# Performance work log

Measured on AMD Instinct MI355X. Metric: run time of the kernel, lower is better.

## Reference

```python
import jax, jax.numpy as jnp
import numpy as np

BN_EPS = 1e-5

def _bn_relu(x, gamma, beta):
    # training-mode BatchNorm1d: biased batch stats over (B, N) per channel
    mean = x.mean(axis=(0, 2), keepdims=True)
    var = x.var(axis=(0, 2), keepdims=True)
    xn = (x - mean) * jax.lax.rsqrt(var + BN_EPS)
    return jax.nn.relu(xn * gamma[None, :, None] + beta[None, :, None])


def setup_inputs() -> dict:
    key = jax.random.key(0)
    ks = jax.random.split(key, 12)
    B, n1, n2, c1, c2 = 16, 4096, 1024, 128, 256
    in_ch, mlp = c1 + c2, [256, 128]
    xyz1 = jax.random.uniform(ks[0], (B, n1, 3), dtype=jnp.float32)
    xyz2 = jax.random.uniform(ks[1], (B, n2, 3), dtype=jnp.float32)
    feat1 = jax.random.normal(ks[2], (B, c1, n1), dtype=jnp.float32)
    feat2 = jax.random.normal(ks[3], (B, c2, n2), dtype=jnp.float32)
    # Conv1d(k=1) weights as (out, in) matrices; kaiming-ish scale
    w0 = jax.random.normal(ks[4], (mlp[0], in_ch), dtype=jnp.float32) / np.sqrt(in_ch)
    b0 = jnp.zeros((mlp[0],), jnp.float32)
    g0 = jnp.ones((mlp[0],), jnp.float32)
    be0 = jnp.zeros((mlp[0],), jnp.float32)
    w1 = jax.random.normal(ks[5], (mlp[1], mlp[0]), dtype=jnp.float32) / np.sqrt(mlp[0])
    b1 = jnp.zeros((mlp[1],), jnp.float32)
    g1 = jnp.ones((mlp[1],), jnp.float32)
    be1 = jnp.zeros((mlp[1],), jnp.float32)
    return {"xyz1": xyz1, "xyz2": xyz2, "feat1": feat1, "feat2": feat2,
            "w0": w0, "b0": b0, "g0": g0, "be0": be0,
            "w1": w1, "b1": b1, "g1": g1, "be1": be1}


def reference(xyz1, xyz2, feat1, feat2, w0, b0, g0, be0, w1, b1, g1, be1):
    # three_nn_interpolate: squared pairwise dists (B, n1, n2)
    d = jnp.sum((xyz1[:, :, None, :] - xyz2[:, None, :, :]) ** 2, axis=-1)
    neg_d3, idx3 = jax.lax.top_k(-d, 3)          # 3 smallest dists
    d3 = -neg_d3                                  # (B, n1, 3)
    w = 1.0 / (d3 + 1e-8)
    w = w / jnp.sum(w, axis=-1, keepdims=True)
    # gather feat2 at knn indices: (B, c2, n1, 3)
    gathered = jnp.take_along_axis(feat2[:, :, None, :], idx3[:, None, :, :], axis=3)
    interp = jnp.sum(gathered * w[:, None, :, :], axis=-1)  # (B, c2, n1)

    x = jnp.concatenate([feat1, interp], axis=1)            # (B, c1+c2, n1)
    x = _bn_relu(jnp.einsum('oc,bcn->bon', w0, x) + b0[None, :, None], g0, be0)
    x = _bn_relu(jnp.einsum('oc,bcn->bon', w1, x) + b1[None, :, None], g1, be1)
    return x
```

## Files before the change

kernel.cpp:

```cpp
#include <hip/hip_runtime.h>
#include <hip/hip_bf16.h>

typedef unsigned short u16;
typedef __attribute__((ext_vector_type(8))) __bf16 bf16x8;
typedef __attribute__((ext_vector_type(4))) float floatx4;

#define B_   16
#define N1_  4096
#define N2_  1024
#define C1_  128
#define C2_  256
#define CIN_ 384
#define CM_  256
#define CO_  128

__device__ __forceinline__ u16 f2bf(float f) {
  unsigned u = __float_as_uint(f);
  u = (u + 0x7fffu + ((u >> 16) & 1u)) >> 16;
  return (u16)u;
}
__device__ __forceinline__ float bf2f(u16 h) {
  return __uint_as_float(((unsigned)h) << 16);
}

union U128 { uint4 u; bf16x8 v; u16 s[8]; };

__device__ __forceinline__ bf16x8 ldfrag(const u16* p) {
  U128 x; x.u = *(const uint4*)p; return x.v;
}
__device__ __forceinline__ uint4 pack8(const u16* h) {
  uint4 u;
  u.x = (unsigned)h[0] | ((unsigned)h[1] << 16);
  u.y = (unsigned)h[2] | ((unsigned)h[3] << 16);
  u.z = (unsigned)h[4] | ((unsigned)h[5] << 16);
  u.w = (unsigned)h[6] | ((unsigned)h[7] << 16);
  return u;
}


__global__ __launch_bounds__(256) void castw_kernel(
    const float* __restrict__ w0, const float* __restrict__ w1,
    u16* __restrict__ w0b, u16* __restrict__ w1b)
{
  int i = blockIdx.x * 256 + threadIdx.x;
  if (i < 12288) {
    int m = i / 48, kc = i % 48;
    const float* p = w0 + m * CIN_ + kc * 8;
    u16 h8[8];
    #pragma unroll
    for (int j = 0; j < 8; ++j) h8[j] = f2bf(p[j]);
    int mt = m >> 4, col = m & 15, kt = kc >> 2, quad = kc & 3;
    *(uint4*)(w0b + ((mt*12 + kt)*512 + (quad*16 + col)*8)) = pack8(h8);
  } else {
    int i2 = i - 12288;
    int m = i2 >> 5, kc = i2 & 31;
    const float* p = w1 + m * CM_ + kc * 8;
    u16 h8[8];
    #pragma unroll
    for (int j = 0; j < 8; ++j) h8[j] = f2bf(p[j]);
    int mt = m >> 4, col = m & 15, kt = kc >> 2, quad = kc & 3;
    *(uint4*)(w1b + ((mt*8 + kt)*512 + (quad*16 + col)*8)) = pack8(h8);
  }
}

__global__ __launch_bounds__(256) void knn_part_kernel(
    const float* __restrict__ xyz1, const float* __restrict__ xyz2,
    float* __restrict__ pd, int* __restrict__ pi)
{
  __shared__ float4 sp[256];
  int b = blockIdx.y;
  int chunk = blockIdx.z;
  int t = threadIdx.x;
  const float* p2 = xyz2 + ((size_t)b * N2_ + chunk * 256) * 3;
  sp[t] = make_float4(p2[t*3], p2[t*3+1], p2[t*3+2], 0.f);
  __syncthreads();
  int i = blockIdx.x * 256 + t;
  const float* p1 = xyz1 + ((size_t)b * N1_ + i) * 3;
  float x = p1[0], y = p1[1], z = p1[2];
  float d0 = 1e30f, d1 = 1e30f, d2 = 1e30f;
  int i0 = 0, i1 = 0, i2 = 0;
  int jbase = chunk * 256;
  #pragma unroll 4
  for (int j = 0; j < 256; ++j) {
    float4 p = sp[j];
    float dx = x - p.x, dy = y - p.y, dz = z - p.z;
    float d = dx*dx + dy*dy + dz*dz;
    if (d < d2) {
      if (d < d0)      { d2=d1; i2=i1; d1=d0; i1=i0; d0=d; i0=jbase+j; }
      else if (d < d1) { d2=d1; i2=i1; d1=d;  i1=jbase+j; }
      else             { d2=d;  i2=jbase+j; }
    }
  }
  int o = chunk*65536 + b*4096 + i;
  pd[o] = d0; pd[o + 262144] = d1; pd[o + 524288] = d2;
  pi[o] = i0; pi[o + 262144] = i1; pi[o + 524288] = i2;
}

__global__ __launch_bounds__(256) void knn_merge_kernel(
    const float* __restrict__ pd, const int* __restrict__ pi,
    int* __restrict__ idx_out, float* __restrict__ w_out)
{
  int p = blockIdx.x * 256 + threadIdx.x;
  float d0 = 1e30f, d1 = 1e30f, d2 = 1e30f;
  int i0 = 0, i1 = 0, i2 = 0;
  #pragma unroll
  for (int c = 0; c < 4; ++c) {
    int o = c*65536 + p;
    #pragma unroll
    for (int k = 0; k < 3; ++k) {
      float d = pd[o + k*262144];
      int ix = pi[o + k*262144];
      if (d < d2) {
        if (d < d0)      { d2=d1; i2=i1; d1=d0; i1=i0; d0=d; i0=ix; }
        else if (d < d1) { d2=d1; i2=i1; d1=d;  i1=ix; }
        else             { d2=d;  i2=ix; }
      }
    }
  }
  float w0 = 1.f/(d0+1e-8f), w1 = 1.f/(d1+1e-8f), w2 = 1.f/(d2+1e-8f);
  float inv = 1.f/(w0+w1+w2);
  idx_out[p]          = i0;
  idx_out[p +  65536] = i1;
  idx_out[p + 131072] = i2;
  w_out[p]            = w0*inv;
  w_out[p +  65536]   = w1*inv;
  w_out[p + 131072]   = w2*inv;
}

__global__ __launch_bounds__(256) void tr2_kernel(
    const float* __restrict__ feat2, u16* __restrict__ feat2Tb)
{
  __shared__ float sA[64][257];
  int b = blockIdx.y;
  int n0 = blockIdx.x * 64;
  int t = threadIdx.x;
  #pragma unroll
  for (int j = 0; j < 16; ++j) {
    int flat4 = t + j * 256;
    int c = flat4 >> 4, nn4 = (flat4 & 15) * 4;
    float4 v = *(const float4*)(feat2 + ((size_t)b*C2_ + c)*N2_ + n0 + nn4);
    sA[nn4+0][c] = v.x; sA[nn4+1][c] = v.y; sA[nn4+2][c] = v.z; sA[nn4+3][c] = v.w;
  }
  __syncthreads();
  int nn = t & 63, chunk = t >> 6;
  u16* dst = feat2Tb + ((size_t)b*N2_ + n0 + nn)*C2_ + chunk*64;
  #pragma unroll
  for (int g = 0; g < 8; ++g) {
    u16 h8[8];
    #pragma unroll
    for (int j = 0; j < 8; ++j) h8[j] = f2bf(sA[nn][chunk*64 + g*8 + j]);
    *(uint4*)(dst + g*8) = pack8(h8);
  }
}

__global__ __launch_bounds__(256) void prep1_kernel(
    const float* __restrict__ feat1, u16* __restrict__ xcatT)
{
  __shared__ float sA[64][133];
  int b = blockIdx.y;
  int n0 = blockIdx.x * 64;
  int t = threadIdx.x;
  #pragma unroll
  for (int j = 0; j < 8; ++j) {
    int flat4 = t + j * 256;
    int c = flat4 >> 4, nn4 = (flat4 & 15) * 4;
    float4 v = *(const float4*)(feat1 + ((size_t)b*C1_ + c)*N1_ + n0 + nn4);
    sA[nn4+0][c] = v.x; sA[nn4+1][c] = v.y; sA[nn4+2][c] = v.z; sA[nn4+3][c] = v.w;
  }
  __syncthreads();
  int nn = t & 63, chunk = t >> 6;
  int n = n0 + nn, nt = n >> 4, col = n & 15;
  u16* tb = xcatT + ((size_t)b*256 + nt)*12*512;
  #pragma unroll
  for (int g = 0; g < 4; ++g) {
    int c0 = chunk*32 + g*8;
    u16 h8[8];
    #pragma unroll
    for (int j = 0; j < 8; ++j) h8[j] = f2bf(sA[nn][c0 + j]);
    *(uint4*)(tb + (size_t)chunk*512 + (g*16 + col)*8) = pack8(h8);
  }
}

__global__ __launch_bounds__(256) void interp2_kernel(
    const u16* __restrict__ feat2Tb, const int* __restrict__ idx_in,
    const float* __restrict__ w_in, u16* __restrict__ xcatT)
{
  int b = blockIdx.y;
  int p0 = blockIdx.x * 64;
  int t = threadIdx.x;
  int seg = t & 31;
  int pl  = t >> 5;
  #pragma unroll 2
  for (int pass = 0; pass < 8; ++pass) {
    int n = p0 + pass*8 + pl;
    int base = b*N1_ + n;
    int i0 = idx_in[base], i1 = idx_in[base + 65536], i2 = idx_in[base + 131072];
    float w0 = w_in[base], w1 = w_in[base + 65536], w2 = w_in[base + 131072];
    const u16* fb = feat2Tb + (size_t)b*N2_*C2_ + seg*8;
    U128 a, c, d;
    a.u = *(const uint4*)(fb + (size_t)i0*C2_);
    c.u = *(const uint4*)(fb + (size_t)i1*C2_);
    d.u = *(const uint4*)(fb + (size_t)i2*C2_);
    u16 h8[8];
    #pragma unroll
    for (int j = 0; j < 8; ++j)
      h8[j] = f2bf(w0*bf2f(a.s[j]) + w1*bf2f(c.s[j]) + w2*bf2f(d.s[j]));
    int nt = n >> 4, col = n & 15;
    int kt = 4 + (seg >> 2), quad = seg & 3;
    *(uint4*)(xcatT + (((size_t)b*256 + nt)*12 + kt)*512 + (quad*16 + col)*8) = pack8(h8);
  }
}

__global__ __launch_bounds__(256) void gemm1_mfma(
    const u16* __restrict__ xcatT, const u16* __restrict__ w0b,
    const float* __restrict__ b0p, u16* __restrict__ y0T,
    float* __restrict__ p0)
{
  __shared__ float ps[4][64][2];
  int t = threadIdx.x;
  int wave = t >> 6, lane = t & 63;
  int col = lane & 15, quad = lane >> 4;
  int wm = wave >> 1, wn = wave & 1;
  int b = blockIdx.y;
  int mtb = blockIdx.z*8 + wm*4;
  int ntb = blockIdx.x*8 + wn*4;

  const u16* ap = w0b + lane*8;
  const u16* bp = xcatT + ((size_t)(b*256 + ntb)*12)*512 + lane*8;

  floatx4 acc[4][4] = {};
  bf16x8 af[4], bf[4], afn[4], bfn[4];
  #pragma unroll
  for (int i = 0; i < 4; ++i) {
    af[i] = ldfrag(ap + (size_t)((mtb+i)*12)*512);
    bf[i] = ldfrag(bp + (size_t)(i*12)*512);
  }
  #pragma unroll 1
  for (int kt = 1; kt < 12; ++kt) {
    #pragma unroll
    for (int i = 0; i < 4; ++i) afn[i] = ldfrag(ap + (size_t)((mtb+i)*12 + kt)*512);
    #pragma unroll
    for (int i = 0; i < 4; ++i) bfn[i] = ldfrag(bp + (size_t)(i*12 + kt)*512);
    #pragma unroll
    for (int mt = 0; mt < 4; ++mt)
      #pragma unroll
      for (int nt = 0; nt < 4; ++nt)
        acc[mt][nt] = __builtin_amdgcn_mfma_f32_16x16x32_bf16(af[mt], bf[nt], acc[mt][nt], 0, 0, 0);
    #pragma unroll
    for (int i = 0; i < 4; ++i) { af[i] = afn[i]; bf[i] = bfn[i]; }
  }
  #pragma unroll
  for (int mt = 0; mt < 4; ++mt)
    #pragma unroll
    for (int nt = 0; nt < 4; ++nt)
      acc[mt][nt] = __builtin_amdgcn_mfma_f32_16x16x32_bf16(af[mt], bf[nt], acc[mt][nt], 0, 0, 0);

  int m0 = blockIdx.z*128 + wm*64;
  #pragma unroll
  for (int mt = 0; mt < 4; ++mt) {
    float4 bias4 = *(const float4*)(b0p + m0 + mt*16 + quad*4);
    float bia[4] = {bias4.x, bias4.y, bias4.z, bias4.w};
    int kt_out = (m0 >> 5) + (mt >> 1);
    int quad_out = ((mt & 1) << 1) | (quad >> 1);
    int j0 = (quad & 1) * 4;
    float s[4] = {}, q[4] = {};
    #pragma unroll
    for (int nt = 0; nt < 4; ++nt) {
      int nt_g = ntb + nt;
      u16 h[4];
      #pragma unroll
      for (int r = 0; r < 4; ++r) {
        float v = acc[mt][nt][r] + bia[r];
        u16 hh = f2bf(v);
        float vr = bf2f(hh);
        h[r] = hh; s[r] += vr; q[r] += vr*vr;
      }
      *(ushort4*)(y0T + (((size_t)b*256 + nt_g)*8 + kt_out)*512 + (quad_out*16 + col)*8 + j0)
          = make_ushort4(h[0], h[1], h[2], h[3]);
    }
    #pragma unroll
    for (int r = 0; r < 4; ++r) {
      float ss = s[r], qq = q[r];
      #pragma unroll
      for (int msk = 1; msk < 16; msk <<= 1) { ss += __shfl_xor(ss, msk); qq += __shfl_xor(qq, msk); }
      if (col == 0) {
        ps[wave][mt*16 + quad*4 + r][0] = ss;
        ps[wave][mt*16 + quad*4 + r][1] = qq;
      }
    }
  }
  __syncthreads();
  {
    int c = t >> 1, k = t & 1;
    int wbase = (c >> 6) * 2, ch = c & 63;
    float v = ps[wbase][ch][k] + ps[wbase+1][ch][k];
    size_t l = (size_t)blockIdx.z*512 + blockIdx.y*32 + blockIdx.x;
    p0[l*256 + t] = v;
  }
}

__global__ __launch_bounds__(256) void stats_kernel(
    const float* __restrict__ p, const float* __restrict__ g,
    const float* __restrict__ be, float* __restrict__ scale,
    float* __restrict__ shift, int half_split)
{
  int c = blockIdx.x, t = threadIdx.x;
  size_t base = half_split ? ((size_t)(c >> 7) * 512 * 256 + (size_t)(c & 127) * 2)
                           : ((size_t)c * 2);
  float s = 0.f, q = 0.f;
  #pragma unroll
  for (int i = 0; i < 2; ++i) {
    float2 v = *(const float2*)(p + base + (size_t)(t + i*256) * 256);
    s += v.x; q += v.y;
  }
  #pragma unroll
  for (int m = 1; m < 64; m <<= 1) { s += __shfl_xor(s, m); q += __shfl_xor(q, m); }
  __shared__ float2 red[4];
  if ((t & 63) == 0) red[t >> 6] = make_float2(s, q);
  __syncthreads();
  if (t == 0) {
    float ss = red[0].x + red[1].x + red[2].x + red[3].x;
    float qq = red[0].y + red[1].y + red[2].y + red[3].y;
    float mu  = ss * (1.f/65536.f);
    float var = qq * (1.f/65536.f) - mu*mu;
    float a = g[c] * rsqrtf(var + 1e-5f);
    scale[c] = a; shift[c] = be[c] - mu*a;
  }
}

__global__ __launch_bounds__(256) void gemm2_mfma(
    const u16* __restrict__ y0T, const u16* __restrict__ w1b,
    const float* __restrict__ b1p,
    const float* __restrict__ scale0, const float* __restrict__ shift0,
    float* __restrict__ out, float* __restrict__ p1)
{
  __shared__ float a0s[CM_], bb0s[CM_];
  __shared__ float ps[4][64][2];
  int t = threadIdx.x;
  a0s[t] = scale0[t]; bb0s[t] = shift0[t];
  __syncthreads();
  int wave = t >> 6, lane = t & 63;
  int col = lane & 15, quad = lane >> 4;
  int wm = wave >> 1, wn = wave & 1;
  int b = blockIdx.y;
  int mtb = wm*4;
  int ntb = blockIdx.x*8 + wn*4;

  const u16* ap = w1b + lane*8;
  const u16* bp = y0T + ((size_t)(b*256 + ntb)*8)*512 + lane*8;

  floatx4 acc[4][4] = {};
  bf16x8 af[4], afn[4];
  U128 braw[4], brawn[4];
  #pragma unroll
  for (int i = 0; i < 4; ++i) {
    af[i] = ldfrag(ap + (size_t)((mtb+i)*8)*512);
    braw[i].u = *(const uint4*)(bp + (size_t)(i*8)*512);
  }
  #pragma unroll 1
  for (int kt = 1; kt < 8; ++kt) {
    #pragma unroll
    for (int i = 0; i < 4; ++i) afn[i] = ldfrag(ap + (size_t)((mtb+i)*8 + kt)*512);
    #pragma unroll
    for (int i = 0; i < 4; ++i) brawn[i].u = *(const uint4*)(bp + (size_t)(i*8 + kt)*512);
    int c0 = (kt-1)*32 + quad*8;
    float4 av0 = *(const float4*)&a0s[c0], av1 = *(const float4*)&a0s[c0+4];
    float4 bv0 = *(const float4*)&bb0s[c0], bv1 = *(const float4*)&bb0s[c0+4];
    float av[8] = {av0.x,av0.y,av0.z,av0.w,av1.x,av1.y,av1.z,av1.w};
    float bv[8] = {bv0.x,bv0.y,bv0.z,bv0.w,bv1.x,bv1.y,bv1.z,bv1.w};
    bf16x8 bfv[4];
    #pragma unroll
    for (int i = 0; i < 4; ++i) {
      u16 h8[8];
      #pragma unroll
      for (int j = 0; j < 8; ++j)
        h8[j] = f2bf(fmaxf(fmaf(bf2f(braw[i].s[j]), av[j], bv[j]), 0.f));
      U128 x; x.u = pack8(h8); bfv[i] = x.v;
    }
    #pragma unroll
    for (int mt = 0; mt < 4; ++mt)
      #pragma unroll
      for (int nt = 0; nt < 4; ++nt)
        acc[mt][nt] = __builtin_amdgcn_mfma_f32_16x16x32_bf16(af[mt], bfv[nt], acc[mt][nt], 0, 0, 0);
    #pragma unroll
    for (int i = 0; i < 4; ++i) { af[i] = afn[i]; braw[i] = brawn[i]; }
  }
  {
    int c0 = 7*32 + quad*8;
    float4 av0 = *(const float4*)&a0s[c0], av1 = *(const float4*)&a0s[c0+4];
    float4 bv0 = *(const float4*)&bb0s[c0], bv1 = *(const float4*)&bb0s[c0+4];
    float av[8] = {av0.x,av0.y,av0.z,av0.w,av1.x,av1.y,av1.z,av1.w};
    float bv[8] = {bv0.x,bv0.y,bv0.z,bv0.w,bv1.x,bv1.y,bv1.z,bv1.w};
    bf16x8 bfv[4];
    #pragma unroll
    for (int i = 0; i < 4; ++i) {
      u16 h8[8];
      #pragma unroll
      for (int j = 0; j < 8; ++j)
        h8[j] = f2bf(fmaxf(fmaf(bf2f(braw[i].s[j]), av[j], bv[j]), 0.f));
      U128 x; x.u = pack8(h8); bfv[i] = x.v;
    }
    #pragma unroll
    for (int mt = 0; mt < 4; ++mt)
      #pragma unroll
      for (int nt = 0; nt < 4; ++nt)
        acc[mt][nt] = __builtin_amdgcn_mfma_f32_16x16x32_bf16(af[mt], bfv[nt], acc[mt][nt], 0, 0, 0);
  }

  int m0 = wm*64;
  int n0 = blockIdx.x*128 + wn*64;
  #pragma unroll
  for (int mt = 0; mt < 4; ++mt) {
    float4 bias4 = *(const float4*)(b1p + m0 + mt*16 + quad*4);
    float bia[4] = {bias4.x, bias4.y, bias4.z, bias4.w};
    float s[4] = {}, q[4] = {};
    #pragma unroll
    for (int nt = 0; nt < 4; ++nt) {
      int n = n0 + nt*16 + col;
      #pragma unroll
      for (int r = 0; r < 4; ++r) {
        float v = acc[mt][nt][r] + bia[r];
        out[((size_t)b*CO_ + m0 + mt*16 + quad*4 + r)*N1_ + n] = v;
        s[r] += v; q[r] += v*v;
      }
    }
    #pragma unroll
    for (int r = 0; r < 4; ++r) {
      float ss = s[r], qq = q[r];
      #pragma unroll
      for (int msk = 1; msk < 16; msk <<= 1) { ss += __shfl_xor(ss, msk); qq += __shfl_xor(qq, msk); }
      if (col == 0) {
        ps[wave][mt*16 + quad*4 + r][0] = ss;
        ps[wave][mt*16 + quad*4 + r][1] = qq;
      }
    }
  }
  __syncthreads();
  {
    int c = t >> 1, k = t & 1;
    int wbase = (c >> 6) * 2, ch = c & 63;
    float v = ps[wbase][ch][k] + ps[wbase+1][ch][k];
    size_t l = (size_t)blockIdx.y*32 + blockIdx.x;
    p1[l*256 + t] = v;
  }
}

__global__ __launch_bounds__(256) void bnrelu_kernel(
    float* __restrict__ out, const float* __restrict__ scale1, const float* __restrict__ shift1)
{
  int idx = blockIdx.x * 256 + threadIdx.x;
  int c = (idx >> 10) & (CO_ - 1);
  float a = scale1[c];
  float bb = shift1[c];
  float4 v = ((const float4*)out)[idx];
  v.x = fmaxf(fmaf(v.x, a, bb), 0.f);
  v.y = fmaxf(fmaf(v.y, a, bb), 0.f);
  v.z = fmaxf(fmaf(v.z, a, bb), 0.f);
  v.w = fmaxf(fmaf(v.w, a, bb), 0.f);
  ((float4*)out)[idx] = v;
}

extern "C" void kernel_launch(void* const* d_in, const int* in_sizes, int n_in,
                              void* d_out, int out_size, void* d_ws, size_t ws_size,
                              hipStream_t stream)
{
  const float* xyz1  = (const float*)d_in[0];
  const float* xyz2  = (const float*)d_in[1];
  const float* feat1 = (const float*)d_in[2];
  const float* feat2 = (const float*)d_in[3];
  const float* w0    = (const float*)d_in[4];
  const float* b0    = (const float*)d_in[5];
  const float* g0    = (const float*)d_in[6];
  const float* be0   = (const float*)d_in[7];
  const float* w1    = (const float*)d_in[8];
  const float* b1    = (const float*)d_in[9];
  const float* g1    = (const float*)d_in[10];
  const float* be1   = (const float*)d_in[11];
  float* out = (float*)d_out;
  char* ws = (char*)d_ws;

  u16*   xcatT   = (u16*)ws;
  float* knn_pd  = (float*)ws;
  int*   knn_pi  = (int*)(ws + 3145728);
  u16*   y0T     = (u16*)(ws + 50331648);
  u16*   feat2Tb = (u16*)(ws + 50331648);
  u16*   w0b     = (u16*)(ws + 83886080);
  u16*   w1b     = (u16*)(ws + 84082688);
  int*   idx_buf = (int*)(ws + 84148224);
  float* w_buf   = (float*)(ws + 84934656);
  float* p0      = (float*)(ws + 85721088);
  float* p1      = (float*)(ws + 86769664);
  float* scale0  = (float*)(ws + 87293952);
  float* shift0  = scale0 + 256;
  float* scale1  = scale0 + 512;
  float* shift1  = scale0 + 640;

  castw_kernel    <<<64,              256, 0, stream>>>(w0, w1, w0b, w1b);
  knn_part_kernel <<<dim3(16,16,4),   256, 0, stream>>>(xyz1, xyz2, knn_pd, knn_pi);
  knn_merge_kernel<<<256,             256, 0, stream>>>(knn_pd, knn_pi, idx_buf, w_buf);
  tr2_kernel      <<<dim3(16,16),     256, 0, stream>>>(feat2, feat2Tb);
  prep1_kernel    <<<dim3(64,16),     256, 0, stream>>>(feat1, xcatT);
  interp2_kernel  <<<dim3(64,16),     256, 0, stream>>>(feat2Tb, idx_buf, w_buf, xcatT);
  gemm1_mfma      <<<dim3(32,16,2),   256, 0, stream>>>(xcatT, w0b, b0, y0T, p0);
  stats_kernel    <<<256,             256, 0, stream>>>(p0, g0, be0, scale0, shift0, 1);
  gemm2_mfma      <<<dim3(32,16),     256, 0, stream>>>(y0T, w1b, b1, scale0, shift0, out, p1);
  stats_kernel    <<<128,             256, 0, stream>>>(p1, g1, be1, scale1, shift1, 0);
  bnrelu_kernel   <<<8192,            256, 0, stream>>>(out, scale1, shift1);
}
```

Before: 251.7 us.

## Restructure KNN into 8 chunks with 4 points per thread, fuse small kernels

The KNN partial kernel now splits xyz2 into 8 chunks of 128 and has each thread process 4 query points with branchless top-3 insertion, so each shared-memory load is reused across 4 points. The merge kernel is widened to combine 8 partial lists. The weight-cast work rides along as an extra block column in the KNN launch, and the feat1 transpose and interpolation kernels are merged into one launch split by block index. The aim is to cut launch count and raise ILP in the distance loop, at the cost of twice as much partial-result traffic and more registers per thread.

```diff
diff --git a/kernel.cpp b/kernel.cpp
--- a/kernel.cpp
+++ b/kernel.cpp
@@ -38,62 +38,74 @@
 }
 
 
-__global__ __launch_bounds__(256) void castw_kernel(
+__global__ __launch_bounds__(256) void knn_part_kernel(
+    const float* __restrict__ xyz1, const float* __restrict__ xyz2,
+    float* __restrict__ pd, int* __restrict__ pi,
     const float* __restrict__ w0, const float* __restrict__ w1,
     u16* __restrict__ w0b, u16* __restrict__ w1b)
 {
-  int i = blockIdx.x * 256 + threadIdx.x;
-  if (i < 12288) {
-    int m = i / 48, kc = i % 48;
-    const float* p = w0 + m * CIN_ + kc * 8;
-    u16 h8[8];
-    #pragma unroll
-    for (int j = 0; j < 8; ++j) h8[j] = f2bf(p[j]);
-    int mt = m >> 4, col = m & 15, kt = kc >> 2, quad = kc & 3;
-    *(uint4*)(w0b + ((mt*12 + kt)*512 + (quad*16 + col)*8)) = pack8(h8);
-  } else {
-    int i2 = i - 12288;
-    int m = i2 >> 5, kc = i2 & 31;
-    const float* p = w1 + m * CM_ + kc * 8;
-    u16 h8[8];
-    #pragma unroll
-    for (int j = 0; j < 8; ++j) h8[j] = f2bf(p[j]);
-    int mt = m >> 4, col = m & 15, kt = kc >> 2, quad = kc & 3;
-    *(uint4*)(w1b + ((mt*8 + kt)*512 + (quad*16 + col)*8)) = pack8(h8);
-  }
-}
-
-__global__ __launch_bounds__(256) void knn_part_kernel(
-    const float* __restrict__ xyz1, const float* __restrict__ xyz2,
-    float* __restrict__ pd, int* __restrict__ pi)
-{
-  __shared__ float4 sp[256];
-  int b = blockIdx.y;
-  int chunk = blockIdx.z;
+  __shared__ float4 sp[128];
   int t = threadIdx.x;
-  const float* p2 = xyz2 + ((size_t)b * N2_ + chunk * 256) * 3;
-  sp[t] = make_float4(p2[t*3], p2[t*3+1], p2[t*3+2], 0.f);
+  if (blockIdx.x == 4) {
+    int item = (blockIdx.y * 8 + blockIdx.z) * 256 + t;
+    if (item < 12288) {
+      int m = item / 48, kc = item % 48;
+      const float* p = w0 + m * CIN_ + kc * 8;
+      u16 h8[8];
+      #pragma unroll
+      for (int j = 0; j < 8; ++j) h8[j] = f2bf(p[j]);
+      int mt = m >> 4, col = m & 15, kt = kc >> 2, quad = kc & 3;
+      *(uint4*)(w0b + ((mt*12 + kt)*512 + (quad*16 + col)*8)) = pack8(h8);
+    } else if (item < 16384) {
+      int i2 = item - 12288;
+      int m = i2 >> 5, kc = i2 & 31;
+      const float* p = w1 + m * CM_ + kc * 8;
+      u16 h8[8];
+      #pragma unroll
+      for (int j = 0; j < 8; ++j) h8[j] = f2bf(p[j]);
+      int mt = m >> 4, col = m & 15, kt = kc >> 2, quad = kc & 3;
+      *(uint4*)(w1b + ((mt*8 + kt)*512 + (quad*16 + col)*8)) = pack8(h8);
+    }
+    return;
+  }
+  int b = blockIdx.y, chunk = blockIdx.z;
+  const float* p2 = xyz2 + ((size_t)b * N2_ + chunk * 128) * 3;
+  if (t < 128) sp[t] = make_float4(p2[t*3], p2[t*3+1], p2[t*3+2], 0.f);
   __syncthreads();
-  int i = blockIdx.x * 256 + t;
-  const float* p1 = xyz1 + ((size_t)b * N1_ + i) * 3;
-  float x = p1[0], y = p1[1], z = p1[2];
-  float d0 = 1e30f, d1 = 1e30f, d2 = 1e30f;
-  int i0 = 0, i1 = 0, i2 = 0;
-  int jbase = chunk * 256;
-  #pragma unroll 4
-  for (int j = 0; j < 256; ++j) {
-    float4 p = sp[j];
-    float dx = x - p.x, dy = y - p.y, dz = z - p.z;
-    float d = dx*dx + dy*dy + dz*dz;
-    if (d < d2) {
-      if (d < d0)      { d2=d1; i2=i1; d1=d0; i1=i0; d0=d; i0=jbase+j; }
-      else if (d < d1) { d2=d1; i2=i1; d1=d;  i1=jbase+j; }
-      else             { d2=d;  i2=jbase+j; }
-    }
-  }
-  int o = chunk*65536 + b*4096 + i;
-  pd[o] = d0; pd[o + 262144] = d1; pd[o + 524288] = d2;
-  pi[o] = i0; pi[o + 262144] = i1; pi[o + 524288] = i2;
+  int pbase = blockIdx.x * 1024 + t;
+  float px[4], py[4], pz[4];
+  float d0[4], d1[4], d2[4];
+  int   i0[4], i1[4], i2[4];
+  #pragma unroll
+  for (int k = 0; k < 4; ++k) {
+    const float* q = xyz1 + ((size_t)b * N1_ + pbase + k*256) * 3;
+    px[k] = q[0]; py[k] = q[1]; pz[k] = q[2];
+    d0[k] = 1e30f; d1[k] = 1e30f; d2[k] = 1e30f;
+    i0[k] = 0; i1[k] = 0; i2[k] = 0;
+  }
+  int jb = chunk * 128;
+  for (int j = 0; j < 128; ++j) {
+    float4 c = sp[j];
+    int jj = jb + j;
+    #pragma unroll
+    for (int k = 0; k < 4; ++k) {
+      float dx = px[k] - c.x, dy = py[k] - c.y, dz = pz[k] - c.z;
+      float d = fmaf(dx, dx, fmaf(dy, dy, dz*dz));
+      bool c2 = d < d2[k], c1 = d < d1[k], c0 = d < d0[k];
+      d2[k] = c1 ? d1[k] : (c2 ? d  : d2[k]);
+      i2[k] = c1 ? i1[k] : (c2 ? jj : i2[k]);
+      d1[k] = c0 ? d0[k] : (c1 ? d  : d1[k]);
+      i1[k] = c0 ? i0[k] : (c1 ? jj : i1[k]);
+      d0[k] = c0 ? d  : d0[k];
+      i0[k] = c0 ? jj : i0[k];
+    }
+  }
+  #pragma unroll
+  for (int k = 0; k < 4; ++k) {
+    int o = chunk*65536 + b*4096 + pbase + k*256;
+    pd[o] = d0[k]; pd[o + 524288] = d1[k]; pd[o + 1048576] = d2[k];
+    pi[o] = i0[k]; pi[o + 524288] = i1[k]; pi[o + 1048576] = i2[k];
+  }
 }
 
 __global__ __launch_bounds__(256) void knn_merge_kernel(
@@ -104,12 +116,12 @@
   float d0 = 1e30f, d1 = 1e30f, d2 = 1e30f;
   int i0 = 0, i1 = 0, i2 = 0;
   #pragma unroll
-  for (int c = 0; c < 4; ++c) {
+  for (int c = 0; c < 8; ++c) {
     int o = c*65536 + p;
     #pragma unroll
     for (int k = 0; k < 3; ++k) {
-      float d = pd[o + k*262144];
-      int ix = pi[o + k*262144];
+      float d = pd[o + k*524288];
+      int ix = pi[o + k*524288];
       if (d < d2) {
         if (d < d0)      { d2=d1; i2=i1; d1=d0; i1=i0; d0=d; i0=ix; }
         else if (d < d1) { d2=d1; i2=i1; d1=d;  i1=ix; }
@@ -153,61 +165,58 @@
   }
 }
 
-__global__ __launch_bounds__(256) void prep1_kernel(
-    const float* __restrict__ feat1, u16* __restrict__ xcatT)
+__global__ __launch_bounds__(256) void prep_fused_kernel(
+    const float* __restrict__ feat1, const u16* __restrict__ feat2Tb,
+    const int* __restrict__ idx_in, const float* __restrict__ w_in,
+    u16* __restrict__ xcatT)
 {
   __shared__ float sA[64][133];
   int b = blockIdx.y;
-  int n0 = blockIdx.x * 64;
   int t = threadIdx.x;
-  #pragma unroll
-  for (int j = 0; j < 8; ++j) {
-    int flat4 = t + j * 256;
-    int c = flat4 >> 4, nn4 = (flat4 & 15) * 4;
-    float4 v = *(const float4*)(feat1 + ((size_t)b*C1_ + c)*N1_ + n0 + nn4);
-    sA[nn4+0][c] = v.x; sA[nn4+1][c] = v.y; sA[nn4+2][c] = v.z; sA[nn4+3][c] = v.w;
-  }
-  __syncthreads();
-  int nn = t & 63, chunk = t >> 6;
-  int n = n0 + nn, nt = n >> 4, col = n & 15;
-  u16* tb = xcatT + ((size_t)b*256 + nt)*12*512;
-  #pragma unroll
-  for (int g = 0; g < 4; ++g) {
-    int c0 = chunk*32 + g*8;
-    u16 h8[8];
-    #pragma unroll
-    for (int j = 0; j < 8; ++j) h8[j] = f2bf(sA[nn][c0 + j]);
-    *(uint4*)(tb + (size_t)chunk*512 + (g*16 + col)*8) = pack8(h8);
-  }
-}
-
-__global__ __launch_bounds__(256) void interp2_kernel(
-    const u16* __restrict__ feat2Tb, const int* __restrict__ idx_in,
-    const float* __restrict__ w_in, u16* __restrict__ xcatT)
-{
-  int b = blockIdx.y;
-  int p0 = blockIdx.x * 64;
-  int t = threadIdx.x;
-  int seg = t & 31;
-  int pl  = t >> 5;
-  #pragma unroll 2
-  for (int pass = 0; pass < 8; ++pass) {
-    int n = p0 + pass*8 + pl;
-    int base = b*N1_ + n;
-    int i0 = idx_in[base], i1 = idx_in[base + 65536], i2 = idx_in[base + 131072];
-    float w0 = w_in[base], w1 = w_in[base + 65536], w2 = w_in[base + 131072];
-    const u16* fb = feat2Tb + (size_t)b*N2_*C2_ + seg*8;
-    U128 a, c, d;
-    a.u = *(const uint4*)(fb + (size_t)i0*C2_);
-    c.u = *(const uint4*)(fb + (size_t)i1*C2_);
-    d.u = *(const uint4*)(fb + (size_t)i2*C2_);
-    u16 h8[8];
-    #pragma unroll
-    for (int j = 0; j < 8; ++j)
-      h8[j] = f2bf(w0*bf2f(a.s[j]) + w1*bf2f(c.s[j]) + w2*bf2f(d.s[j]));
-    int nt = n >> 4, col = n & 15;
-    int kt = 4 + (seg >> 2), quad = seg & 3;
-    *(uint4*)(xcatT + (((size_t)b*256 + nt)*12 + kt)*512 + (quad*16 + col)*8) = pack8(h8);
+  if (blockIdx.x < 64) {
+    int n0 = blockIdx.x * 64;
+    #pragma unroll
+    for (int j = 0; j < 8; ++j) {
+      int flat4 = t + j * 256;
+      int c = flat4 >> 4, nn4 = (flat4 & 15) * 4;
+      float4 v = *(const float4*)(feat1 + ((size_t)b*C1_ + c)*N1_ + n0 + nn4);
+      sA[nn4+0][c] = v.x; sA[nn4+1][c] = v.y; sA[nn4+2][c] = v.z; sA[nn4+3][c] = v.w;
+    }
+    __syncthreads();
+    int nn = t & 63, chunk = t >> 6;
+    int n = n0 + nn, nt = n >> 4, col = n & 15;
+    u16* tb = xcatT + ((size_t)b*256 + nt)*12*512;
+    #pragma unroll
+    for (int g = 0; g < 4; ++g) {
+      int c0 = chunk*32 + g*8;
+      u16 h8[8];
+      #pragma unroll
+      for (int j = 0; j < 8; ++j) h8[j] = f2bf(sA[nn][c0 + j]);
+      *(uint4*)(tb + (size_t)chunk*512 + (g*16 + col)*8) = pack8(h8);
+    }
+  } else {
+    int p0 = (blockIdx.x - 64) * 64;
+    int seg = t & 31;
+    int pl  = t >> 5;
+    #pragma unroll 2
+    for (int pass = 0; pass < 8; ++pass) {
+      int n = p0 + pass*8 + pl;
+      int base = b*N1_ + n;
+      int i0 = idx_in[base], i1 = idx_in[base + 65536], i2 = idx_in[base + 131072];
+      float w0 = w_in[base], w1 = w_in[base + 65536], w2 = w_in[base + 131072];
+      const u16* fb = feat2Tb + (size_t)b*N2_*C2_ + seg*8;
+      U128 a, c, d;
+      a.u = *(const uint4*)(fb + (size_t)i0*C2_);
+      c.u = *(const uint4*)(fb + (size_t)i1*C2_);
+      d.u = *(const uint4*)(fb + (size_t)i2*C2_);
+      u16 h8[8];
+      #pragma unroll
+      for (int j = 0; j < 8; ++j)
+        h8[j] = f2bf(w0*bf2f(a.s[j]) + w1*bf2f(c.s[j]) + w2*bf2f(d.s[j]));
+      int nt = n >> 4, col = n & 15;
+      int kt = 4 + (seg >> 2), quad = seg & 3;
+      *(uint4*)(xcatT + (((size_t)b*256 + nt)*12 + kt)*512 + (quad*16 + col)*8) = pack8(h8);
+    }
   }
 }
 
@@ -481,7 +490,7 @@
 
   u16*   xcatT   = (u16*)ws;
   float* knn_pd  = (float*)ws;
-  int*   knn_pi  = (int*)(ws + 3145728);
+  int*   knn_pi  = (int*)(ws + 6291456);
   u16*   y0T     = (u16*)(ws + 50331648);
   u16*   feat2Tb = (u16*)(ws + 50331648);
   u16*   w0b     = (u16*)(ws + 83886080);
@@ -495,12 +504,10 @@
   float* scale1  = scale0 + 512;
   float* shift1  = scale0 + 640;
 
-  castw_kernel    <<<64,              256, 0, stream>>>(w0, w1, w0b, w1b);
-  knn_part_kernel <<<dim3(16,16,4),   256, 0, stream>>>(xyz1, xyz2, knn_pd, knn_pi);
+  knn_part_kernel <<<dim3(5,16,8),    256, 0, stream>>>(xyz1, xyz2, knn_pd, knn_pi, w0, w1, w0b, w1b);
   knn_merge_kernel<<<256,             256, 0, stream>>>(knn_pd, knn_pi, idx_buf, w_buf);
   tr2_kernel      <<<dim3(16,16),     256, 0, stream>>>(feat2, feat2Tb);
-  prep1_kernel    <<<dim3(64,16),     256, 0, stream>>>(feat1, xcatT);
-  interp2_kernel  <<<dim3(64,16),     256, 0, stream>>>(feat2Tb, idx_buf, w_buf, xcatT);
+  prep_fused_kernel<<<dim3(128,16),   256, 0, stream>>>(feat1, feat2Tb, idx_buf, w_buf, xcatT);
   gemm1_mfma      <<<dim3(32,16,2),   256, 0, stream>>>(xcatT, w0b, b0, y0T, p0);
   stats_kernel    <<<256,             256, 0, stream>>>(p0, g0, be0, scale0, shift0, 1);
   gemm2_mfma      <<<dim3(32,16),     256, 0, stream>>>(y0T, w1b, b1, scale0, shift0, out, p1);
```

Result: slower. 275.8 us (+9.6%).
